# Performance work log

Hardware: AMD Instinct MI355X
Metric: run time of the kernel (lower is better)

Reference implementation:

```python
import jax, jax.numpy as jnp
import numpy as np

D = 512       # input_embedding_dimensions
H = 2         # num_heads
HD = D // H   # head_dim = 256
B = 16
S = 1194      # max_sequence_length


def setup_inputs() -> dict:
    key = jax.random.key(0)
    k1, k2, k3, k4, k5 = jax.random.split(key, 5)
    scale_in = 1.0 / np.sqrt(D)
    return {
        "positional_embeddings": jax.random.normal(k1, (B, S, D), dtype=jnp.float32),
        "W_qkv": jax.random.uniform(k2, (D, 3 * D), minval=-scale_in, maxval=scale_in, dtype=jnp.float32),
        "b_qkv": jax.random.uniform(k3, (3 * D,), minval=-scale_in, maxval=scale_in, dtype=jnp.float32),
        "W_out": jax.random.uniform(k4, (D, D), minval=-scale_in, maxval=scale_in, dtype=jnp.float32),
        "b_out": jax.random.uniform(k5, (D,), minval=-scale_in, maxval=scale_in, dtype=jnp.float32),
    }


def reference(positional_embeddings, W_qkv, b_qkv, W_out, b_out):
    x = positional_embeddings              # [B, S, D]
    b, s, _ = x.shape
    qkv = x @ W_qkv + b_qkv                # [B, S, 3D]
    q, k, v = jnp.split(qkv, 3, axis=-1)

    def split_heads(t):
        return t.reshape(b, s, H, HD).transpose(0, 2, 1, 3)  # [B, H, S, HD]

    q, k, v = split_heads(q), split_heads(k), split_heads(v)
    scores = jnp.einsum("bhqd,bhkd->bhqk", q, k) / jnp.sqrt(jnp.float32(HD))
    causal = jnp.tril(jnp.ones((s, s), dtype=bool))          # [S, S]
    scores = jnp.where(causal[None, None, :, :], scores, -jnp.inf)
    att = jax.nn.softmax(scores, axis=-1)                    # [B, H, S, S]
    out = jnp.einsum("bhqk,bhkd->bhqd", att, v)              # [B, H, S, HD]
    out = out.transpose(0, 2, 1, 3).reshape(b, s, D)         # [B, S, D]
    return out @ W_out + b_out
```

## Files before the change

### kernel.cpp

```cpp
#include <hip/hip_runtime.h>
#include <stdint.h>

#define D_    512
#define H_    2
#define HD_   256
#define B_    16
#define S_    1194
#define MTOK  19104
#define MPAD  19200
#define SPAD  1216
#define NQKV  1536
#define NT_   19
#define LOG2E 1.44269504088896340736f

typedef unsigned short u16;
typedef __attribute__((ext_vector_type(8))) short bf16x8;
typedef __attribute__((ext_vector_type(4))) float f32x4;

__device__ inline u16 f2bf(float x) {
  union { float f; unsigned u; } c; c.f = x;
  unsigned r = c.u + 0x7fffu + ((c.u >> 16) & 1u);
  return (u16)(r >> 16);
}

__device__ inline void async_copy16(void* lds, const void* g) {
  __builtin_amdgcn_global_load_lds(
      (__attribute__((address_space(1))) void*)(g),
      (__attribute__((address_space(3))) void*)(lds),
      16, 0, 0);
}

__global__ void convert_kernel(const float* __restrict__ X,
                               const float* __restrict__ Wqkv,
                               const float* __restrict__ Wout,
                               u16* __restrict__ Xf,
                               u16* __restrict__ Wqf,
                               u16* __restrict__ Wof) {
  const int NXG = MPAD * 64;
  const int NQG = 12 * 8 * 16 * 64;
  const int NOG = 4 * 8 * 16 * 64;
  const int TOT = NXG + NQG + NOG;
  int stride = gridDim.x * blockDim.x;
  for (int g = blockIdx.x * blockDim.x + threadIdx.x; g < TOT; g += stride) {
    if (g < NXG) {
      int lane = g & 63, f = (g >> 6) & 15, kt = (g >> 10) & 7, mt = g >> 13;
      int i = mt * 128 + (f & 7) * 16 + (lane & 15);
      int k = kt * 64 + (f >> 3) * 32 + (lane >> 4) * 8;
      bf16x8 o;
      if (i < MTOK) {
        f32x4 v0 = *(const f32x4*)&X[(size_t)i * 512 + k];
        f32x4 v1 = *(const f32x4*)&X[(size_t)i * 512 + k + 4];
#pragma unroll
        for (int e = 0; e < 4; ++e) { o[e] = (short)f2bf(v0[e]); o[4 + e] = (short)f2bf(v1[e]); }
      } else {
#pragma unroll
        for (int e = 0; e < 8; ++e) o[e] = 0;
      }
      *(bf16x8*)&Xf[(size_t)g * 8] = o;
    } else if (g < NXG + NQG) {
      int gg = g - NXG;
      int lane = gg & 63, f = (gg >> 6) & 15, kt = (gg >> 10) & 7, nt = gg >> 13;
      int j = nt * 128 + (f & 7) * 16 + (lane & 15);
      int k = kt * 64 + (f >> 3) * 32 + (lane >> 4) * 8;
      bf16x8 o;
#pragma unroll
      for (int e = 0; e < 8; ++e) o[e] = (short)f2bf(Wqkv[(size_t)(k + e) * NQKV + j]);
      *(bf16x8*)&Wqf[(size_t)gg * 8] = o;
    } else {
      int gg = g - NXG - NQG;
      int lane = gg & 63, f = (gg >> 6) & 15, kt = (gg >> 10) & 7, nt = gg >> 13;
      int j = nt * 128 + (f & 7) * 16 + (lane & 15);
      int k = kt * 64 + (f >> 3) * 32 + (lane >> 4) * 8;
      bf16x8 o;
#pragma unroll
      for (int e = 0; e < 8; ++e) o[e] = (short)f2bf(Wout[(size_t)(k + e) * 512 + j]);
      *(bf16x8*)&Wof[(size_t)gg * 8] = o;
    }
  }
}

template<int MODE>
__global__ __launch_bounds__(256, 2) void gemm_kernel(
    const u16* __restrict__ Af, const u16* __restrict__ Bf,
    const float* __restrict__ bias, int nb,
    u16* __restrict__ Qb, u16* __restrict__ Kf, u16* __restrict__ Vf,
    float* __restrict__ Cout)
{
  __shared__ u16 ldsA[2][16 * 512];
  __shared__ u16 ldsB[2][16 * 512];

  const int t  = threadIdx.x;
  const int l  = t & 63;
  const int w  = t >> 6;
  const int lr = l >> 4, lc = l & 15;

  const int nwg = gridDim.x;
  const int qq = nwg >> 3, rr8 = nwg & 7;
  const int xcd = blockIdx.x & 7, off = blockIdx.x >> 3;
  const int wgid = (xcd < rr8 ? xcd * (qq + 1) : rr8 * (qq + 1) + (xcd - rr8) * qq) + off;
  const int m0 = (wgid / nb) * 128;
  const int n0 = (wgid % nb) * 128;

  const u16* pA = Af + ((size_t)(m0 >> 7) * 128 + w) * 512 + l * 8;
  const u16* pB = Bf + ((size_t)(n0 >> 7) * 128 + w) * 512 + l * 8;

  f32x4 acc[4][4] = {};

#pragma unroll
  for (int c = 0; c < 4; ++c) {
    async_copy16(&ldsA[0][(c * 4 + w) * 512], pA + c * 2048);
    async_copy16(&ldsB[0][(c * 4 + w) * 512], pB + c * 2048);
  }
  __syncthreads();

  for (int kt = 0; kt < 8; ++kt) {
    const int cur = kt & 1;
    if (kt < 7) {
      const u16* qA = pA + (kt + 1) * 8192;
      const u16* qB = pB + (kt + 1) * 8192;
#pragma unroll
      for (int c = 0; c < 4; ++c) {
        async_copy16(&ldsA[cur ^ 1][(c * 4 + w) * 512], qA + c * 2048);
        async_copy16(&ldsB[cur ^ 1][(c * 4 + w) * 512], qB + c * 2048);
      }
    }
#pragma unroll
    for (int kk = 0; kk < 2; ++kk) {
      bf16x8 af[4], bfr[4];
#pragma unroll
      for (int m = 0; m < 4; ++m)
        af[m] = *(bf16x8*)&ldsA[cur][((kk * 8 + (w >> 1) * 4 + m) * 64 + l) * 8];
#pragma unroll
      for (int n = 0; n < 4; ++n)
        bfr[n] = *(bf16x8*)&ldsB[cur][((kk * 8 + (w & 1) * 4 + n) * 64 + l) * 8];
      __builtin_amdgcn_s_setprio(1);
#pragma unroll
      for (int m = 0; m < 4; ++m)
#pragma unroll
        for (int n = 0; n < 4; ++n)
          acc[m][n] = __builtin_amdgcn_mfma_f32_16x16x32_bf16(af[m], bfr[n], acc[m][n], 0, 0, 0);
      __builtin_amdgcn_s_setprio(0);
    }
    __syncthreads();
  }

  int jv[4]; float bj[4];
#pragma unroll
  for (int n = 0; n < 4; ++n) { jv[n] = n0 + (w & 1) * 64 + n * 16 + lc; bj[n] = bias[jv[n]]; }

#pragma unroll
  for (int m = 0; m < 4; ++m) {
#pragma unroll
    for (int r = 0; r < 4; ++r) {
      int i = m0 + (w >> 1) * 64 + m * 16 + lr * 4 + r;
      if (i >= MTOK) continue;
      if (MODE == 0) {
        int b = i / S_, s = i - b * S_;
        int st = s >> 6, nfs = (s >> 4) & 3, lis = s & 15;
        int kk2 = (s >> 5) & 1, lhs = (s >> 3) & 3, es = s & 7;
#pragma unroll
        for (int n = 0; n < 4; ++n) {
          int j = jv[n];
          int which = j >> 9, h = (j >> 8) & 1, d = j & 255;
          int bh = b * H_ + h;
          u16 v = f2bf(acc[m][n][r] + bj[n]);
          if (which == 0) {
            Qb[((size_t)(bh * SPAD + s)) * HD_ + d] = v;
          } else if (which == 1) {
            Kf[(((size_t)(bh * NT_ + st)) * 32 + (d >> 5) * 4 + nfs) * 512 +
               (((d >> 3) & 3) * 16 + lis) * 8 + (d & 7)] = v;
          } else {
            Vf[(((size_t)(bh * NT_ + st)) * 32 + kk2 * 16 + (d >> 4)) * 512 +
               (lhs * 16 + (d & 15)) * 8 + es] = v;
          }
        }
      } else {
#pragma unroll
        for (int n = 0; n < 4; ++n)
          Cout[(size_t)i * D_ + jv[n]] = acc[m][n][r] + bj[n];
      }
    }
  }
}

__global__ __launch_bounds__(256) void attn_kernel(
    const u16* __restrict__ Qb, const u16* __restrict__ Kf,
    const u16* __restrict__ Vf, u16* __restrict__ Obf)
{
  __shared__ u16 ldsK[32 * 64 * 8];
  __shared__ u16 ldsV[32 * 64 * 8];
  __shared__ u16 ldsP[4][16 * 72];

  const int id   = blockIdx.x;
  const int xcd  = id & 7;
  const int slot = id >> 3;
  const int bh   = xcd + 8 * (slot / NT_);
  const int qt   = (NT_ - 1) - (slot % NT_);
  const int q0 = qt * 64;
  const int t  = threadIdx.x, l = t & 63, w = t >> 6;
  const int lr = l >> 4, lc = l & 15;

  bf16x8 qf[8];
  const u16* qbase = Qb + (size_t)(bh * SPAD + q0 + w * 16 + lc) * HD_ + lr * 8;
#pragma unroll
  for (int kb = 0; kb < 8; ++kb)
    qf[kb] = *(const bf16x8*)(qbase + kb * 32);

  f32x4 oacc[16] = {};
  float mrow[4] = {-1e30f, -1e30f, -1e30f, -1e30f};
  float lsum[4] = {0.f, 0.f, 0.f, 0.f};

  for (int kt = 0; kt <= qt; ++kt) {
    const u16* kbase = Kf + (((size_t)(bh * NT_ + kt)) * 32 + w) * 512 + l * 8;
    const u16* vbase = Vf + (((size_t)(bh * NT_ + kt)) * 32 + w) * 512 + l * 8;
    __syncthreads();
#pragma unroll
    for (int c = 0; c < 8; ++c) {
      async_copy16(&ldsK[(c * 4 + w) * 512], kbase + c * 2048);
      async_copy16(&ldsV[(c * 4 + w) * 512], vbase + c * 2048);
    }
    __syncthreads();

    const int kv0 = kt * 64;
    f32x4 sacc[4] = {};
#pragma unroll
    for (int kb = 0; kb < 8; ++kb) {
#pragma unroll
      for (int nf = 0; nf < 4; ++nf) {
        bf16x8 kf = *(bf16x8*)&ldsK[((kb * 4 + nf) * 64 + l) * 8];
        sacc[nf] = __builtin_amdgcn_mfma_f32_16x16x32_bf16(qf[kb], kf, sacc[nf], 0, 0, 0);
      }
    }

    float sval[4][4];
    float pm[4] = {-1e30f, -1e30f, -1e30f, -1e30f};
#pragma unroll
    for (int nf = 0; nf < 4; ++nf) {
      int col = kv0 + nf * 16 + lc;
#pragma unroll
      for (int r = 0; r < 4; ++r) {
        int row = q0 + w * 16 + lr * 4 + r;
        float v = ((col <= row) && (col < S_)) ? sacc[nf][r] * 0.0625f : -1e30f;
        sval[nf][r] = v;
        pm[r] = fmaxf(pm[r], v);
      }
    }
#pragma unroll
    for (int r = 0; r < 4; ++r) {
      pm[r] = fmaxf(pm[r], __shfl_xor(pm[r], 1));
      pm[r] = fmaxf(pm[r], __shfl_xor(pm[r], 2));
      pm[r] = fmaxf(pm[r], __shfl_xor(pm[r], 4));
      pm[r] = fmaxf(pm[r], __shfl_xor(pm[r], 8));
      float mn = fmaxf(mrow[r], pm[r]);
      float sc = exp2f((mrow[r] - mn) * LOG2E);
      mrow[r] = mn;
      lsum[r] *= sc;
#pragma unroll
      for (int nf = 0; nf < 16; ++nf) oacc[nf][r] *= sc;
    }
#pragma unroll
    for (int nf = 0; nf < 4; ++nf) {
#pragma unroll
      for (int r = 0; r < 4; ++r) {
        float p = exp2f((sval[nf][r] - mrow[r]) * LOG2E);
        lsum[r] += p;
        ldsP[w][(lr * 4 + r) * 72 + nf * 16 + lc] = f2bf(p);
      }
    }

#pragma unroll
    for (int kk = 0; kk < 2; ++kk) {
      bf16x8 pf = *(bf16x8*)&ldsP[w][lc * 72 + kk * 32 + lr * 8];
#pragma unroll
      for (int nf = 0; nf < 16; ++nf) {
        bf16x8 vf = *(bf16x8*)&ldsV[((kk * 16 + nf) * 64 + l) * 8];
        oacc[nf] = __builtin_amdgcn_mfma_f32_16x16x32_bf16(pf, vf, oacc[nf], 0, 0, 0);
      }
    }
  }

  float inv[4];
#pragma unroll
  for (int r = 0; r < 4; ++r) {
    float s = lsum[r];
    s += __shfl_xor(s, 1); s += __shfl_xor(s, 2);
    s += __shfl_xor(s, 4); s += __shfl_xor(s, 8);
    inv[r] = 1.0f / s;
  }
  const int b = bh >> 1, h = bh & 1;
#pragma unroll
  for (int r = 0; r < 4; ++r) {
    int q = q0 + w * 16 + lr * 4 + r;
    if (q < S_) {
      int i = b * S_ + q;
      int it = i >> 7, mf = (i >> 4) & 7, li = i & 15;
#pragma unroll
      for (int nf = 0; nf < 16; ++nf) {
        int j = h * HD_ + nf * 16 + lc;
        size_t addr = (((size_t)(it * 8 + (j >> 6))) * 16 + ((j >> 5) & 1) * 8 + mf) * 512 +
                      (((j >> 3) & 3) * 16 + li) * 8 + (j & 7);
        Obf[addr] = f2bf(oacc[nf][r] * inv[r]);
      }
    }
  }
}

extern "C" void kernel_launch(void* const* d_in, const int* in_sizes, int n_in,
                              void* d_out, int out_size, void* d_ws, size_t ws_size,
                              hipStream_t stream) {
  const float* X    = (const float*)d_in[0];
  const float* Wqkv = (const float*)d_in[1];
  const float* bqkv = (const float*)d_in[2];
  const float* Wout = (const float*)d_in[3];
  const float* bout = (const float*)d_in[4];
  float* out = (float*)d_out;

  char* ws = (char*)d_ws;
  u16* Xf  = (u16*)ws;  ws += (size_t)MPAD * D_ * 2;
  u16* Wqf = (u16*)ws;  ws += (size_t)NQKV * D_ * 2;
  u16* Wof = (u16*)ws;  ws += (size_t)D_ * D_ * 2;
  u16* Qb  = (u16*)ws;  ws += (size_t)B_ * H_ * SPAD * HD_ * 2;
  u16* Kf  = (u16*)ws;  ws += (size_t)B_ * H_ * SPAD * HD_ * 2;
  u16* Vf  = (u16*)ws;  ws += (size_t)B_ * H_ * SPAD * HD_ * 2;
  u16* Obf = (u16*)ws;  ws += (size_t)MPAD * D_ * 2;

  convert_kernel<<<2048, 256, 0, stream>>>(X, Wqkv, Wout, Xf, Wqf, Wof);
  gemm_kernel<0><<<1800, 256, 0, stream>>>(Xf, Wqf, bqkv, 12, Qb, Kf, Vf, nullptr);
  attn_kernel<<<608, 256, 0, stream>>>(Qb, Kf, Vf, Obf);
  gemm_kernel<1><<<600, 256, 0, stream>>>(Obf, Wof, bout, 4, nullptr, nullptr, nullptr, out);
}
```

Before: 182.4 us.

## Double Q tile per block to 128 rows and double-buffer K/V loads

The attention kernel now processes 128 query rows per block, two 16-row sub-tiles per wave, so each K/V tile loaded into LDS is reused across twice as many MFMA operations. K/V loads for the next tile are issued asynchronously into a second LDS buffer while the current tile is computed, which removes one barrier per iteration. The grid drops from 608 to 320 blocks. Register pressure and LDS use roughly double, and the last diagonal tile does more masked, wasted work.

```diff
diff --git a/kernel.cpp b/kernel.cpp
--- a/kernel.cpp
+++ b/kernel.cpp
@@ -11,6 +11,7 @@
 #define SPAD  1216
 #define NQKV  1536
 #define NT_   19
+#define QT_   10
 #define LOG2E 1.44269504088896340736f
 
 typedef unsigned short u16;
@@ -183,123 +184,154 @@
   }
 }
 
-__global__ __launch_bounds__(256) void attn_kernel(
+__global__ __launch_bounds__(256, 1) void attn_kernel(
     const u16* __restrict__ Qb, const u16* __restrict__ Kf,
     const u16* __restrict__ Vf, u16* __restrict__ Obf)
 {
-  __shared__ u16 ldsK[32 * 64 * 8];
-  __shared__ u16 ldsV[32 * 64 * 8];
-  __shared__ u16 ldsP[4][16 * 72];
+  __shared__ u16 ldsK[2][32 * 512];
+  __shared__ u16 ldsV[2][32 * 512];
+  __shared__ u16 ldsP[4][32 * 72];
 
   const int id   = blockIdx.x;
   const int xcd  = id & 7;
   const int slot = id >> 3;
-  const int bh   = xcd + 8 * (slot / NT_);
-  const int qt   = (NT_ - 1) - (slot % NT_);
-  const int q0 = qt * 64;
+  const int bh   = xcd + 8 * (slot / QT_);
+  const int qt   = (QT_ - 1) - (slot % QT_);
+  const int q0   = qt * 128;
+  const int nkv  = min(2 * qt + 2, NT_);
   const int t  = threadIdx.x, l = t & 63, w = t >> 6;
   const int lr = l >> 4, lc = l & 15;
-
-  bf16x8 qf[8];
-  const u16* qbase = Qb + (size_t)(bh * SPAD + q0 + w * 16 + lc) * HD_ + lr * 8;
-#pragma unroll
-  for (int kb = 0; kb < 8; ++kb)
-    qf[kb] = *(const bf16x8*)(qbase + kb * 32);
-
-  f32x4 oacc[16] = {};
-  float mrow[4] = {-1e30f, -1e30f, -1e30f, -1e30f};
-  float lsum[4] = {0.f, 0.f, 0.f, 0.f};
-
-  for (int kt = 0; kt <= qt; ++kt) {
-    const u16* kbase = Kf + (((size_t)(bh * NT_ + kt)) * 32 + w) * 512 + l * 8;
-    const u16* vbase = Vf + (((size_t)(bh * NT_ + kt)) * 32 + w) * 512 + l * 8;
+  const int wq0 = q0 + w * 32;
+
+  bf16x8 qf[2][8];
+#pragma unroll
+  for (int a = 0; a < 2; ++a) {
+    int qr = wq0 + a * 16 + lc; if (qr >= S_) qr = S_ - 1;
+    const u16* qbase = Qb + (size_t)(bh * SPAD + qr) * HD_ + lr * 8;
+#pragma unroll
+    for (int kb = 0; kb < 8; ++kb)
+      qf[a][kb] = *(const bf16x8*)(qbase + kb * 32);
+  }
+
+  f32x4 oacc[2][16] = {};
+  float mrow[2][4], lsum[2][4];
+#pragma unroll
+  for (int a = 0; a < 2; ++a)
+#pragma unroll
+    for (int r = 0; r < 4; ++r) { mrow[a][r] = -1e30f; lsum[a][r] = 0.f; }
+
+  {
+    const u16* kb_ = Kf + (((size_t)(bh * NT_)) * 32 + w) * 512 + l * 8;
+    const u16* vb_ = Vf + (((size_t)(bh * NT_)) * 32 + w) * 512 + l * 8;
+#pragma unroll
+    for (int c = 0; c < 8; ++c) {
+      async_copy16(&ldsK[0][(c * 4 + w) * 512], kb_ + c * 2048);
+      async_copy16(&ldsV[0][(c * 4 + w) * 512], vb_ + c * 2048);
+    }
+  }
+  __syncthreads();
+
+  for (int kt = 0; kt < nkv; ++kt) {
+    const int cur = kt & 1;
+    if (kt + 1 < nkv) {
+      const u16* kb_ = Kf + (((size_t)(bh * NT_ + kt + 1)) * 32 + w) * 512 + l * 8;
+      const u16* vb_ = Vf + (((size_t)(bh * NT_ + kt + 1)) * 32 + w) * 512 + l * 8;
+#pragma unroll
+      for (int c = 0; c < 8; ++c) {
+        async_copy16(&ldsK[cur ^ 1][(c * 4 + w) * 512], kb_ + c * 2048);
+        async_copy16(&ldsV[cur ^ 1][(c * 4 + w) * 512], vb_ + c * 2048);
+      }
+    }
+
+    f32x4 sacc[2][4] = {};
+#pragma unroll
+    for (int kb = 0; kb < 8; ++kb) {
+#pragma unroll
+      for (int nf = 0; nf < 4; ++nf) {
+        bf16x8 kf = *(bf16x8*)&ldsK[cur][((kb * 4 + nf) * 64 + l) * 8];
+        sacc[0][nf] = __builtin_amdgcn_mfma_f32_16x16x32_bf16(qf[0][kb], kf, sacc[0][nf], 0, 0, 0);
+        sacc[1][nf] = __builtin_amdgcn_mfma_f32_16x16x32_bf16(qf[1][kb], kf, sacc[1][nf], 0, 0, 0);
+      }
+    }
+
+    const int kv0 = kt * 64;
+#pragma unroll
+    for (int a = 0; a < 2; ++a) {
+      float sval[4][4];
+      float pm[4] = {-1e30f, -1e30f, -1e30f, -1e30f};
+#pragma unroll
+      for (int nf = 0; nf < 4; ++nf) {
+        int col = kv0 + nf * 16 + lc;
+#pragma unroll
+        for (int r = 0; r < 4; ++r) {
+          int row = wq0 + a * 16 + lr * 4 + r;
+          float v = ((col <= row) && (col < S_)) ? sacc[a][nf][r] * 0.0625f : -1e30f;
+          sval[nf][r] = v;
+          pm[r] = fmaxf(pm[r], v);
+        }
+      }
+#pragma unroll
+      for (int r = 0; r < 4; ++r) {
+        pm[r] = fmaxf(pm[r], __shfl_xor(pm[r], 1));
+        pm[r] = fmaxf(pm[r], __shfl_xor(pm[r], 2));
+        pm[r] = fmaxf(pm[r], __shfl_xor(pm[r], 4));
+        pm[r] = fmaxf(pm[r], __shfl_xor(pm[r], 8));
+        float mn = fmaxf(mrow[a][r], pm[r]);
+        float sc = exp2f((mrow[a][r] - mn) * LOG2E);
+        mrow[a][r] = mn;
+        lsum[a][r] *= sc;
+#pragma unroll
+        for (int nf = 0; nf < 16; ++nf) oacc[a][nf][r] *= sc;
+      }
+#pragma unroll
+      for (int nf = 0; nf < 4; ++nf) {
+#pragma unroll
+        for (int r = 0; r < 4; ++r) {
+          float p = exp2f((sval[nf][r] - mrow[a][r]) * LOG2E);
+          lsum[a][r] += p;
+          ldsP[w][(a * 16 + lr * 4 + r) * 72 + nf * 16 + lc] = f2bf(p);
+        }
+      }
+    }
+
+#pragma unroll
+    for (int kk = 0; kk < 2; ++kk) {
+      bf16x8 pf0 = *(bf16x8*)&ldsP[w][(lc) * 72 + kk * 32 + lr * 8];
+      bf16x8 pf1 = *(bf16x8*)&ldsP[w][(16 + lc) * 72 + kk * 32 + lr * 8];
+#pragma unroll
+      for (int nf = 0; nf < 16; ++nf) {
+        bf16x8 vf = *(bf16x8*)&ldsV[cur][((kk * 16 + nf) * 64 + l) * 8];
+        oacc[0][nf] = __builtin_amdgcn_mfma_f32_16x16x32_bf16(pf0, vf, oacc[0][nf], 0, 0, 0);
+        oacc[1][nf] = __builtin_amdgcn_mfma_f32_16x16x32_bf16(pf1, vf, oacc[1][nf], 0, 0, 0);
+      }
+    }
     __syncthreads();
-#pragma unroll
-    for (int c = 0; c < 8; ++c) {
-      async_copy16(&ldsK[(c * 4 + w) * 512], kbase + c * 2048);
-      async_copy16(&ldsV[(c * 4 + w) * 512], vbase + c * 2048);
-    }
-    __syncthreads();
-
-    const int kv0 = kt * 64;
-    f32x4 sacc[4] = {};
-#pragma unroll
-    for (int kb = 0; kb < 8; ++kb) {
-#pragma unroll
-      for (int nf = 0; nf < 4; ++nf) {
-        bf16x8 kf = *(bf16x8*)&ldsK[((kb * 4 + nf) * 64 + l) * 8];
-        sacc[nf] = __builtin_amdgcn_mfma_f32_16x16x32_bf16(qf[kb], kf, sacc[nf], 0, 0, 0);
-      }
-    }
-
-    float sval[4][4];
-    float pm[4] = {-1e30f, -1e30f, -1e30f, -1e30f};
-#pragma unroll
-    for (int nf = 0; nf < 4; ++nf) {
-      int col = kv0 + nf * 16 + lc;
-#pragma unroll
-      for (int r = 0; r < 4; ++r) {
-        int row = q0 + w * 16 + lr * 4 + r;
-        float v = ((col <= row) && (col < S_)) ? sacc[nf][r] * 0.0625f : -1e30f;
-        sval[nf][r] = v;
-        pm[r] = fmaxf(pm[r], v);
-      }
-    }
+  }
+
+  const int b = bh >> 1, h = bh & 1;
+#pragma unroll
+  for (int a = 0; a < 2; ++a) {
+    float inv[4];
 #pragma unroll
     for (int r = 0; r < 4; ++r) {
-      pm[r] = fmaxf(pm[r], __shfl_xor(pm[r], 1));
-      pm[r] = fmaxf(pm[r], __shfl_xor(pm[r], 2));
-      pm[r] = fmaxf(pm[r], __shfl_xor(pm[r], 4));
-      pm[r] = fmaxf(pm[r], __shfl_xor(pm[r], 8));
-      float mn = fmaxf(mrow[r], pm[r]);
-      float sc = exp2f((mrow[r] - mn) * LOG2E);
-      mrow[r] = mn;
-      lsum[r] *= sc;
-#pragma unroll
-      for (int nf = 0; nf < 16; ++nf) oacc[nf][r] *= sc;
-    }
-#pragma unroll
-    for (int nf = 0; nf < 4; ++nf) {
-#pragma unroll
-      for (int r = 0; r < 4; ++r) {
-        float p = exp2f((sval[nf][r] - mrow[r]) * LOG2E);
-        lsum[r] += p;
-        ldsP[w][(lr * 4 + r) * 72 + nf * 16 + lc] = f2bf(p);
-      }
-    }
-
-#pragma unroll
-    for (int kk = 0; kk < 2; ++kk) {
-      bf16x8 pf = *(bf16x8*)&ldsP[w][lc * 72 + kk * 32 + lr * 8];
-#pragma unroll
-      for (int nf = 0; nf < 16; ++nf) {
-        bf16x8 vf = *(bf16x8*)&ldsV[((kk * 16 + nf) * 64 + l) * 8];
-        oacc[nf] = __builtin_amdgcn_mfma_f32_16x16x32_bf16(pf, vf, oacc[nf], 0, 0, 0);
-      }
-    }
-  }
-
-  float inv[4];
-#pragma unroll
-  for (int r = 0; r < 4; ++r) {
-    float s = lsum[r];
-    s += __shfl_xor(s, 1); s += __shfl_xor(s, 2);
-    s += __shfl_xor(s, 4); s += __shfl_xor(s, 8);
-    inv[r] = 1.0f / s;
-  }
-  const int b = bh >> 1, h = bh & 1;
-#pragma unroll
-  for (int r = 0; r < 4; ++r) {
-    int q = q0 + w * 16 + lr * 4 + r;
-    if (q < S_) {
-      int i = b * S_ + q;
-      int it = i >> 7, mf = (i >> 4) & 7, li = i & 15;
-#pragma unroll
-      for (int nf = 0; nf < 16; ++nf) {
-        int j = h * HD_ + nf * 16 + lc;
-        size_t addr = (((size_t)(it * 8 + (j >> 6))) * 16 + ((j >> 5) & 1) * 8 + mf) * 512 +
-                      (((j >> 3) & 3) * 16 + li) * 8 + (j & 7);
-        Obf[addr] = f2bf(oacc[nf][r] * inv[r]);
+      float s = lsum[a][r];
+      s += __shfl_xor(s, 1); s += __shfl_xor(s, 2);
+      s += __shfl_xor(s, 4); s += __shfl_xor(s, 8);
+      inv[r] = 1.0f / s;
+    }
+#pragma unroll
+    for (int r = 0; r < 4; ++r) {
+      int qrow = wq0 + a * 16 + lr * 4 + r;
+      if (qrow < S_) {
+        int i = b * S_ + qrow;
+        int it = i >> 7, mf = (i >> 4) & 7, li = i & 15;
+#pragma unroll
+        for (int nf = 0; nf < 16; ++nf) {
+          int j = h * HD_ + nf * 16 + lc;
+          size_t addr = (((size_t)(it * 8 + (j >> 6))) * 16 + ((j >> 5) & 1) * 8 + mf) * 512 +
+                        (((j >> 3) & 3) * 16 + li) * 8 + (j & 7);
+          Obf[addr] = f2bf(oacc[a][nf][r] * inv[r]);
+        }
       }
     }
   }
@@ -326,6 +358,6 @@
 
   convert_kernel<<<2048, 256, 0, stream>>>(X, Wqkv, Wout, Xf, Wqf, Wof);
   gemm_kernel<0><<<1800, 256, 0, stream>>>(Xf, Wqf, bqkv, 12, Qb, Kf, Vf, nullptr);
-  attn_kernel<<<608, 256, 0, stream>>>(Qb, Kf, Vf, Obf);
+  attn_kernel<<<320, 256, 0, stream>>>(Qb, Kf, Vf, Obf);
   gemm_kernel<1><<<600, 256, 0, stream>>>(Obf, Wof, bout, 4, nullptr, nullptr, nullptr, out);
 }
```

Measured after the change: 231.2 us. +26.8%, slower.

## Double-buffer 32-wide KV tiles in attention with lazy rescale and mask skip

Applied to the files above, without the earlier changes.

The attention loop now uses 32-key KV tiles with two LDS buffers. The next tile's K/V is prefetched asynchronously while the current tile is computed, which removes the load-then-sync stall at the start of each iteration. The K/V scatter layout in the QKV GEMM epilogue is changed to match the new tile size. Tiles lying fully below the diagonal skip the causal mask test. The online-softmax rescale of the output accumulator is skipped unless the running max grows by more than a threshold. s_setprio hints and launch_bounds(256,2) are added around the MFMA blocks. The cost is more loop iterations, each with a barrier, and higher register pressure.

```diff
diff --git a/kernel.cpp b/kernel.cpp
--- a/kernel.cpp
+++ b/kernel.cpp
@@ -10,7 +10,7 @@
 #define MPAD  19200
 #define SPAD  1216
 #define NQKV  1536
-#define NT_   19
+#define NKT   38
 #define LOG2E 1.44269504088896340736f
 
 typedef unsigned short u16;
@@ -156,8 +156,11 @@
       if (i >= MTOK) continue;
       if (MODE == 0) {
         int b = i / S_, s = i - b * S_;
-        int st = s >> 6, nfs = (s >> 4) & 3, lis = s & 15;
-        int kk2 = (s >> 5) & 1, lhs = (s >> 3) & 3, es = s & 7;
+        int stK  = s >> 5;
+        int nfs  = (s >> 4) & 1;
+        int lisK = s & 15;
+        int lvhi = (s >> 3) & 3;
+        int es   = s & 7;
 #pragma unroll
         for (int n = 0; n < 4; ++n) {
           int j = jv[n];
@@ -167,11 +170,11 @@
           if (which == 0) {
             Qb[((size_t)(bh * SPAD + s)) * HD_ + d] = v;
           } else if (which == 1) {
-            Kf[(((size_t)(bh * NT_ + st)) * 32 + (d >> 5) * 4 + nfs) * 512 +
-               (((d >> 3) & 3) * 16 + lis) * 8 + (d & 7)] = v;
+            Kf[(((size_t)(bh * NKT + stK)) * 16 + (d >> 5) * 2 + nfs) * 512 +
+               (((d >> 3) & 3) * 16 + lisK) * 8 + (d & 7)] = v;
           } else {
-            Vf[(((size_t)(bh * NT_ + st)) * 32 + kk2 * 16 + (d >> 4)) * 512 +
-               (lhs * 16 + (d & 15)) * 8 + es] = v;
+            Vf[(((size_t)(bh * NKT + stK)) * 16 + (d >> 4)) * 512 +
+               (lvhi * 16 + (d & 15)) * 8 + es] = v;
           }
         }
       } else {
@@ -183,25 +186,27 @@
   }
 }
 
-__global__ __launch_bounds__(256) void attn_kernel(
+__global__ __launch_bounds__(256, 2) void attn_kernel(
     const u16* __restrict__ Qb, const u16* __restrict__ Kf,
     const u16* __restrict__ Vf, u16* __restrict__ Obf)
 {
-  __shared__ u16 ldsK[32 * 64 * 8];
-  __shared__ u16 ldsV[32 * 64 * 8];
-  __shared__ u16 ldsP[4][16 * 72];
+  __shared__ u16 ldsK[2][16 * 512];
+  __shared__ u16 ldsV[2][16 * 512];
+  __shared__ u16 ldsP[4][16 * 36];
 
   const int id   = blockIdx.x;
   const int xcd  = id & 7;
   const int slot = id >> 3;
-  const int bh   = xcd + 8 * (slot / NT_);
-  const int qt   = (NT_ - 1) - (slot % NT_);
-  const int q0 = qt * 64;
+  const int bh   = xcd + 8 * (slot / 19);
+  const int qt   = 18 - (slot % 19);
+  const int q0   = qt * 64;
+  const int nkv  = 2 * qt + 2;
   const int t  = threadIdx.x, l = t & 63, w = t >> 6;
   const int lr = l >> 4, lc = l & 15;
+  const int wq0 = q0 + w * 16;
 
   bf16x8 qf[8];
-  const u16* qbase = Qb + (size_t)(bh * SPAD + q0 + w * 16 + lc) * HD_ + lr * 8;
+  const u16* qbase = Qb + (size_t)(bh * SPAD + wq0 + lc) * HD_ + lr * 8;
 #pragma unroll
   for (int kb = 0; kb < 8; ++kb)
     qf[kb] = *(const bf16x8*)(qbase + kb * 32);
@@ -210,39 +215,64 @@
   float mrow[4] = {-1e30f, -1e30f, -1e30f, -1e30f};
   float lsum[4] = {0.f, 0.f, 0.f, 0.f};
 
-  for (int kt = 0; kt <= qt; ++kt) {
-    const u16* kbase = Kf + (((size_t)(bh * NT_ + kt)) * 32 + w) * 512 + l * 8;
-    const u16* vbase = Vf + (((size_t)(bh * NT_ + kt)) * 32 + w) * 512 + l * 8;
-    __syncthreads();
-#pragma unroll
-    for (int c = 0; c < 8; ++c) {
-      async_copy16(&ldsK[(c * 4 + w) * 512], kbase + c * 2048);
-      async_copy16(&ldsV[(c * 4 + w) * 512], vbase + c * 2048);
-    }
-    __syncthreads();
-
-    const int kv0 = kt * 64;
-    f32x4 sacc[4] = {};
+  {
+    const u16* kb_ = Kf + (((size_t)(bh * NKT)) * 16 + w) * 512 + l * 8;
+    const u16* vb_ = Vf + (((size_t)(bh * NKT)) * 16 + w) * 512 + l * 8;
+#pragma unroll
+    for (int c = 0; c < 4; ++c) {
+      async_copy16(&ldsK[0][(c * 4 + w) * 512], kb_ + c * 2048);
+      async_copy16(&ldsV[0][(c * 4 + w) * 512], vb_ + c * 2048);
+    }
+  }
+  __syncthreads();
+
+  for (int kt = 0; kt < nkv; ++kt) {
+    const int cur = kt & 1;
+    if (kt + 1 < nkv) {
+      const u16* kb_ = Kf + (((size_t)(bh * NKT + kt + 1)) * 16 + w) * 512 + l * 8;
+      const u16* vb_ = Vf + (((size_t)(bh * NKT + kt + 1)) * 16 + w) * 512 + l * 8;
+#pragma unroll
+      for (int c = 0; c < 4; ++c) {
+        async_copy16(&ldsK[cur ^ 1][(c * 4 + w) * 512], kb_ + c * 2048);
+        async_copy16(&ldsV[cur ^ 1][(c * 4 + w) * 512], vb_ + c * 2048);
+      }
+    }
+
+    f32x4 sacc[2] = {};
+    __builtin_amdgcn_s_setprio(1);
 #pragma unroll
     for (int kb = 0; kb < 8; ++kb) {
 #pragma unroll
-      for (int nf = 0; nf < 4; ++nf) {
-        bf16x8 kf = *(bf16x8*)&ldsK[((kb * 4 + nf) * 64 + l) * 8];
+      for (int nf = 0; nf < 2; ++nf) {
+        bf16x8 kf = *(bf16x8*)&ldsK[cur][((kb * 2 + nf) * 64 + l) * 8];
         sacc[nf] = __builtin_amdgcn_mfma_f32_16x16x32_bf16(qf[kb], kf, sacc[nf], 0, 0, 0);
       }
     }
-
-    float sval[4][4];
+    __builtin_amdgcn_s_setprio(0);
+
+    const int kv0 = kt * 32;
+    float sval[2][4];
     float pm[4] = {-1e30f, -1e30f, -1e30f, -1e30f};
-#pragma unroll
-    for (int nf = 0; nf < 4; ++nf) {
-      int col = kv0 + nf * 16 + lc;
-#pragma unroll
-      for (int r = 0; r < 4; ++r) {
-        int row = q0 + w * 16 + lr * 4 + r;
-        float v = ((col <= row) && (col < S_)) ? sacc[nf][r] * 0.0625f : -1e30f;
-        sval[nf][r] = v;
-        pm[r] = fmaxf(pm[r], v);
+    if (kv0 + 31 <= wq0) {
+#pragma unroll
+      for (int nf = 0; nf < 2; ++nf)
+#pragma unroll
+        for (int r = 0; r < 4; ++r) {
+          float v = sacc[nf][r] * 0.0625f;
+          sval[nf][r] = v;
+          pm[r] = fmaxf(pm[r], v);
+        }
+    } else {
+#pragma unroll
+      for (int nf = 0; nf < 2; ++nf) {
+        int col = kv0 + nf * 16 + lc;
+#pragma unroll
+        for (int r = 0; r < 4; ++r) {
+          int row = wq0 + lr * 4 + r;
+          float v = ((col <= row) && (col < S_)) ? sacc[nf][r] * 0.0625f : -1e30f;
+          sval[nf][r] = v;
+          pm[r] = fmaxf(pm[r], v);
+        }
       }
     }
 #pragma unroll
@@ -251,32 +281,38 @@
       pm[r] = fmaxf(pm[r], __shfl_xor(pm[r], 2));
       pm[r] = fmaxf(pm[r], __shfl_xor(pm[r], 4));
       pm[r] = fmaxf(pm[r], __shfl_xor(pm[r], 8));
-      float mn = fmaxf(mrow[r], pm[r]);
-      float sc = exp2f((mrow[r] - mn) * LOG2E);
-      mrow[r] = mn;
-      lsum[r] *= sc;
-#pragma unroll
-      for (int nf = 0; nf < 16; ++nf) oacc[nf][r] *= sc;
-    }
-#pragma unroll
-    for (int nf = 0; nf < 4; ++nf) {
+    }
+    bool skip = (pm[0] <= mrow[0] + 8.0f) && (pm[1] <= mrow[1] + 8.0f) &&
+                (pm[2] <= mrow[2] + 8.0f) && (pm[3] <= mrow[3] + 8.0f);
+    if (!__all(skip)) {
+#pragma unroll
+      for (int r = 0; r < 4; ++r) {
+        float mn = fmaxf(mrow[r], pm[r]);
+        float sc = exp2f((mrow[r] - mn) * LOG2E);
+        mrow[r] = mn;
+        lsum[r] *= sc;
+#pragma unroll
+        for (int nf = 0; nf < 16; ++nf) oacc[nf][r] *= sc;
+      }
+    }
+#pragma unroll
+    for (int nf = 0; nf < 2; ++nf)
 #pragma unroll
       for (int r = 0; r < 4; ++r) {
         float p = exp2f((sval[nf][r] - mrow[r]) * LOG2E);
         lsum[r] += p;
-        ldsP[w][(lr * 4 + r) * 72 + nf * 16 + lc] = f2bf(p);
-      }
-    }
-
-#pragma unroll
-    for (int kk = 0; kk < 2; ++kk) {
-      bf16x8 pf = *(bf16x8*)&ldsP[w][lc * 72 + kk * 32 + lr * 8];
-#pragma unroll
-      for (int nf = 0; nf < 16; ++nf) {
-        bf16x8 vf = *(bf16x8*)&ldsV[((kk * 16 + nf) * 64 + l) * 8];
-        oacc[nf] = __builtin_amdgcn_mfma_f32_16x16x32_bf16(pf, vf, oacc[nf], 0, 0, 0);
-      }
-    }
+        ldsP[w][(lr * 4 + r) * 36 + nf * 16 + lc] = f2bf(p);
+      }
+
+    bf16x8 pf = *(bf16x8*)&ldsP[w][lc * 36 + lr * 8];
+    __builtin_amdgcn_s_setprio(1);
+#pragma unroll
+    for (int nf = 0; nf < 16; ++nf) {
+      bf16x8 vf = *(bf16x8*)&ldsV[cur][(nf * 64 + l) * 8];
+      oacc[nf] = __builtin_amdgcn_mfma_f32_16x16x32_bf16(pf, vf, oacc[nf], 0, 0, 0);
+    }
+    __builtin_amdgcn_s_setprio(0);
+    __syncthreads();
   }
 
   float inv[4];
@@ -290,9 +326,9 @@
   const int b = bh >> 1, h = bh & 1;
 #pragma unroll
   for (int r = 0; r < 4; ++r) {
-    int q = q0 + w * 16 + lr * 4 + r;
-    if (q < S_) {
-      int i = b * S_ + q;
+    int qrow = wq0 + lr * 4 + r;
+    if (qrow < S_) {
+      int i = b * S_ + qrow;
       int it = i >> 7, mf = (i >> 4) & 7, li = i & 15;
 #pragma unroll
       for (int nf = 0; nf < 16; ++nf) {
```

Measured after the change: 177.0 us. 1.03x faster.
